# Kernel optimization log

Hardware: AMD Instinct MI355X
Metric: run time of the kernel (lower is better)

Reference implementation:

```python
import jax, jax.numpy as jnp
import numpy as np

TEMPERATURE = 8.0  # sqrt(d_k=64)
NEG_FILL = -1000.0


def setup_inputs() -> dict:
    key = jax.random.key(0)
    k1, k2, k3, k4 = jax.random.split(key, 4)
    B, Lq, Lk, D = 16, 2048, 2048, 64
    q = jax.random.normal(k1, (B, Lq, D), dtype=jnp.float32)
    k = jax.random.normal(k2, (B, Lk, D), dtype=jnp.float32)
    v = jax.random.normal(k3, (B, Lk, D), dtype=jnp.float32)
    pad_mask = jax.random.randint(k4, (B, Lk), 0, 2).astype(bool)
    return {"q": q, "k": k, "v": v, "pad_mask": pad_mask}


def reference(q, k, v, pad_mask):
    # scores: [B, Lq, Lk]
    attn = jnp.einsum('bqd,bkd->bqk', q, k) / TEMPERATURE
    # mask padded keys (broadcast over query dim, like pad_mask.unsqueeze(1))
    attn = jnp.where(pad_mask[:, None, :], NEG_FILL, attn)
    attn = jax.nn.softmax(attn, axis=-1)
    # dropout is identity in eval / p=0
    output = jnp.einsum('bqk,bkd->bqd', attn, v)
    return output, attn
```

## Files before the change

kernel.cpp:

```cpp
#include <hip/hip_runtime.h>
#include <hip/hip_bf16.h>

#define BB 16
#define LL 2048
#define DD 64

typedef __attribute__((ext_vector_type(8))) short short8t;
typedef __attribute__((ext_vector_type(4))) float f32x4;
typedef __attribute__((ext_vector_type(4))) unsigned short ushort4t;

__device__ __forceinline__ unsigned short f2bf(float x) {
  union { float f; unsigned int u; } c; c.f = x;
  unsigned int u = c.u;
  u += 0x7fffu + ((u >> 16) & 1u);
  return (unsigned short)(u >> 16);
}

__global__ void cvt_bf16(const float* __restrict__ in, unsigned short* __restrict__ out) {
  int i = (blockIdx.x * 256 + threadIdx.x) * 4;
  float4 v = *(const float4*)(in + i);
  ushort4t o;
  o.x = f2bf(v.x); o.y = f2bf(v.y); o.z = f2bf(v.z); o.w = f2bf(v.w);
  *(ushort4t*)(out + i) = o;
}

__global__ void vtrans(const float* __restrict__ v, unsigned short* __restrict__ vt) {
  __shared__ unsigned short t[64][66];
  int b = blockIdx.x >> 5, j0 = (blockIdx.x & 31) * 64;
  const float* src = v + ((size_t)b * LL + j0) * DD;
#pragma unroll
  for (int i = 0; i < 16; ++i) {
    int lin = i * 256 + threadIdx.x;
    int j = lin >> 6, d = lin & 63;
    t[j][d] = f2bf(src[lin]);
  }
  __syncthreads();
  unsigned short* dst = vt + (size_t)b * DD * LL;
#pragma unroll
  for (int i = 0; i < 16; ++i) {
    int lin = i * 256 + threadIdx.x;
    int d = lin >> 6, j = lin & 63;
    dst[(size_t)d * LL + j0 + j] = t[j][d];
  }
}

__device__ __forceinline__ void async_cp16(const unsigned short* src, unsigned short* dst_lds) {
  __builtin_amdgcn_global_load_lds(
      (const __attribute__((address_space(1))) unsigned int*)src,
      (__attribute__((address_space(3))) unsigned int*)dst_lds, 16, 0, 0);
}

__global__ void __launch_bounds__(256, 2)
attn_main(const unsigned short* __restrict__ Qb, const unsigned short* __restrict__ Kb,
          const unsigned short* __restrict__ VTb, const int* __restrict__ mask,
          float* __restrict__ out, float* __restrict__ attn) {
  __shared__ __align__(16) unsigned short TB[4][10240];
  float* redF = (float*)&TB[0][6144];
  float* rinvF = redF + 256;

  const int tid = threadIdx.x;
  const int w = tid >> 6;
  const int l = tid & 63;
  const int l15 = l & 15;
  const int g = l >> 4;

  const int swzb = (blockIdx.x & 7) * 64 + (blockIdx.x >> 3);
  const int b = swzb >> 5;
  const int q0 = (swzb & 31) << 6;

  unsigned short* K0 = &TB[w][0];
  unsigned short* K1 = &TB[w][2048];
  unsigned short* VB = &TB[w][4096];
  float* PF = (float*)&TB[w][6144];

  const unsigned short* Kbb = Kb + (size_t)b * LL * DD;
  const unsigned short* VTbb = VTb + (size_t)b * DD * LL;
  const int* maskb = mask + b * LL;

  auto loadK = [&](int k0, unsigned short* KB) {
    const unsigned short* gs = Kbb + (size_t)k0 * DD;
#pragma unroll
    for (int i2 = 0; i2 < 4; ++i2) {
      int row = i2 * 8 + (l >> 3);
      int ce = (l & 7) * 8;
      async_cp16(gs + row * 64 + (ce ^ ((row & 3) << 4)), KB + i2 * 512);
    }
  };
  auto loadV = [&](int k0) {
    const unsigned short* gs = VTbb + k0;
#pragma unroll
    for (int i2 = 0; i2 < 4; ++i2) {
      int row = i2 * 16 + (l >> 2);
      int ce = (l & 3) * 8;
      async_cp16(gs + (size_t)row * LL + (ce ^ ((row & 1) << 4)), VB + i2 * 512);
    }
  };

  short8t qf[4][2];
  {
    const unsigned short* qbase = Qb + ((size_t)b * LL + q0 + l15) * DD + 8 * g;
#pragma unroll
    for (int mi = 0; mi < 4; ++mi)
#pragma unroll
      for (int h = 0; h < 2; ++h)
        qf[mi][h] = *(const short8t*)(qbase + mi * 16 * DD + 32 * h);
  }

  float ls[4][4];
#pragma unroll
  for (int mi = 0; mi < 4; ++mi)
#pragma unroll
    for (int r = 0; r < 4; ++r) ls[mi][r] = 0.f;

  auto stepA = [&](int t, int tn, unsigned short* KBc, unsigned short* KBn,
                   int mk0c, int mk1c, int& mk0n, int& mk1n) {
    asm volatile("s_waitcnt vmcnt(0)" ::: "memory");
    loadK(tn * 32, KBn);
    mk0n = maskb[tn * 32 + l15];
    mk1n = maskb[tn * 32 + 16 + l15];

    short8t kf[2][2];
#pragma unroll
    for (int ni = 0; ni < 2; ++ni)
#pragma unroll
      for (int h = 0; h < 2; ++h) {
        int row = 16 * ni + l15;
        int col = (32 * h + 8 * g) ^ ((l15 & 3) << 4);
        kf[ni][h] = *(const short8t*)(KBc + row * 64 + col);
      }

    f32x4 sacc[4][2] = {};
    __builtin_amdgcn_s_setprio(1);
#pragma unroll
    for (int mi = 0; mi < 4; ++mi)
#pragma unroll
      for (int ni = 0; ni < 2; ++ni)
#pragma unroll
        for (int h = 0; h < 2; ++h)
          sacc[mi][ni] = __builtin_amdgcn_mfma_f32_16x16x32_bf16(qf[mi][h], kf[ni][h], sacc[mi][ni], 0, 0, 0);
    __builtin_amdgcn_s_setprio(0);
#pragma unroll
    for (int mi = 0; mi < 4; ++mi)
#pragma unroll
      for (int ni = 0; ni < 2; ++ni) {
        int mk = ni ? mk1c : mk0c;
#pragma unroll
        for (int r = 0; r < 4; ++r) {
          float p = mk ? 0.f : __expf(sacc[mi][ni][r] * 0.125f);
          ls[mi][r] += p;
        }
      }
  };

  {
    loadK(w * 32, K0);
    int a0 = maskb[w * 32 + l15], a1 = maskb[w * 32 + 16 + l15];
    int b0, b1;
    for (int j = 0; j < 8; ++j) {
      int t = w + 8 * j;
      stepA(t, t + 4, K0, K1, a0, a1, b0, b1);
      int t2 = t + 4;
      int tn = (j == 7) ? w : (t2 + 4);
      stepA(t2, tn, K1, K0, b0, b1, a0, a1);
    }
  }

#pragma unroll
  for (int mi = 0; mi < 4; ++mi)
#pragma unroll
    for (int r = 0; r < 4; ++r) {
      float s = ls[mi][r];
      s += __shfl_xor(s, 1);
      s += __shfl_xor(s, 2);
      s += __shfl_xor(s, 4);
      s += __shfl_xor(s, 8);
      if (l15 == 0) redF[w * 64 + 16 * mi + 4 * g + r] = s;
    }
  __syncthreads();
  if (tid < 64)
    rinvF[tid] = 1.0f / (redF[tid] + redF[64 + tid] + redF[128 + tid] + redF[192 + tid]);
  __syncthreads();

  float rinv_[4][4];
#pragma unroll
  for (int mi = 0; mi < 4; ++mi)
#pragma unroll
    for (int r = 0; r < 4; ++r) rinv_[mi][r] = rinvF[16 * mi + 4 * g + r];
  __syncthreads();

  f32x4 oacc[4][4] = {};
  const size_t arow = (size_t)b * LL + q0;
  auto stepB = [&](int t, int tn, const unsigned short* KBc, unsigned short* KBn,
                   int mk0c, int mk1c, int& mk0n, int& mk1n) {
    asm volatile("s_waitcnt vmcnt(8)" ::: "memory");
    const int k0 = t * 32;

    short8t kf[2][2], vf[4];
#pragma unroll
    for (int ni = 0; ni < 2; ++ni)
#pragma unroll
      for (int h = 0; h < 2; ++h) {
        int row = 16 * ni + l15;
        int col = (32 * h + 8 * g) ^ ((l15 & 3) << 4);
        kf[ni][h] = *(const short8t*)(KBc + row * 64 + col);
      }
#pragma unroll
    for (int ni = 0; ni < 4; ++ni)
      vf[ni] = *(const short8t*)(VB + (16 * ni + l15) * 32 + ((8 * g) ^ ((l & 1) << 4)));
    asm volatile("s_waitcnt lgkmcnt(0)" ::: "memory");
    __builtin_amdgcn_sched_barrier(0);

    loadK(tn * 32, KBn);
    mk0n = maskb[tn * 32 + l15];
    mk1n = maskb[tn * 32 + 16 + l15];
    loadV(tn * 32);

    f32x4 sacc[4][2] = {};
    __builtin_amdgcn_s_setprio(1);
#pragma unroll
    for (int mi = 0; mi < 4; ++mi)
#pragma unroll
      for (int ni = 0; ni < 2; ++ni)
#pragma unroll
        for (int h = 0; h < 2; ++h)
          sacc[mi][ni] = __builtin_amdgcn_mfma_f32_16x16x32_bf16(qf[mi][h], kf[ni][h], sacc[mi][ni], 0, 0, 0);
    __builtin_amdgcn_s_setprio(0);

#pragma unroll
    for (int mi = 0; mi < 4; ++mi)
#pragma unroll
      for (int ni = 0; ni < 2; ++ni) {
        int mk = ni ? mk1c : mk0c;
#pragma unroll
        for (int r = 0; r < 4; ++r) {
          float p = mk ? 0.f : __expf(sacc[mi][ni][r] * 0.125f) * rinv_[mi][r];
          PF[(16 * mi + 4 * g + r) * 32 + ((16 * ni + l15) ^ ((g & 1) << 4))] = p;
        }
      }

#pragma unroll
    for (int it = 0; it < 8; ++it) {
      int row = it * 8 + (l >> 3);
      int c4 = (l & 7) * 4;
      f32x4 pv = *(const f32x4*)(PF + row * 32 + (c4 ^ (((row >> 2) & 1) << 4)));
      __builtin_nontemporal_store(pv, (f32x4*)(attn + (arow + row) * LL + k0 + c4));
    }

    short8t pf[4];
#pragma unroll
    for (int mi = 0; mi < 4; ++mi) {
      int qq = 16 * mi + l15;
      const float* src = PF + qq * 32 + ((8 * g) ^ (((l15 >> 2) & 1) << 4));
      float4 pa = *(const float4*)(src);
      float4 pb = *(const float4*)(src + 4);
      short8t f;
      f[0] = (short)f2bf(pa.x); f[1] = (short)f2bf(pa.y);
      f[2] = (short)f2bf(pa.z); f[3] = (short)f2bf(pa.w);
      f[4] = (short)f2bf(pb.x); f[5] = (short)f2bf(pb.y);
      f[6] = (short)f2bf(pb.z); f[7] = (short)f2bf(pb.w);
      pf[mi] = f;
    }
    __builtin_amdgcn_s_setprio(1);
#pragma unroll
    for (int mi = 0; mi < 4; ++mi)
#pragma unroll
      for (int ni = 0; ni < 4; ++ni)
        oacc[mi][ni] = __builtin_amdgcn_mfma_f32_16x16x32_bf16(pf[mi], vf[ni], oacc[mi][ni], 0, 0, 0);
    __builtin_amdgcn_s_setprio(0);
  };

  {
    loadK(w * 32, K0);
    int a0 = maskb[w * 32 + l15], a1 = maskb[w * 32 + 16 + l15];
    loadV(w * 32);
    asm volatile("s_waitcnt vmcnt(0)" ::: "memory");
    int b0, b1;
    for (int j = 0; j < 8; ++j) {
      int t = w + 8 * j;
      stepB(t, t + 4, K0, K1, a0, a1, b0, b1);
      int t2 = t + 4;
      int tn = (j == 7) ? w : (t2 + 4);
      stepB(t2, tn, K1, K0, b0, b1, a0, a1);
    }
  }

  asm volatile("s_waitcnt vmcnt(0)" ::: "memory");

  __syncthreads();
  float* OB = (float*)&TB[0][0];
  if (w) {
#pragma unroll
    for (int mi = 0; mi < 4; ++mi)
#pragma unroll
      for (int ni = 0; ni < 4; ++ni)
#pragma unroll
        for (int r = 0; r < 4; ++r)
          OB[(w - 1) * 4096 + (16 * mi + 4 * g + r) * 64 + 16 * ni + l15] = oacc[mi][ni][r];
  }
  __syncthreads();
  if (w == 0) {
#pragma unroll
    for (int mi = 0; mi < 4; ++mi)
#pragma unroll
      for (int ni = 0; ni < 4; ++ni)
#pragma unroll
        for (int r = 0; r < 4; ++r) {
          int pos = (16 * mi + 4 * g + r) * 64 + 16 * ni + l15;
          OB[12288 + pos] = oacc[mi][ni][r] + OB[pos] + OB[4096 + pos] + OB[8192 + pos];
        }
  }
  __syncthreads();
#pragma unroll
  for (int it = 0; it < 4; ++it) {
    int lin = it * 256 + tid;
    int row = lin >> 4;
    int c4 = (lin & 15) * 4;
    float4 o4 = *(const float4*)(OB + 12288 + row * 64 + c4);
    *(float4*)(out + ((size_t)(b * LL + q0 + row)) * DD + c4) = o4;
  }
}

extern "C" void kernel_launch(void* const* d_in, const int* in_sizes, int n_in,
                              void* d_out, int out_size, void* d_ws, size_t ws_size,
                              hipStream_t stream) {
  const float* q = (const float*)d_in[0];
  const float* k = (const float*)d_in[1];
  const float* v = (const float*)d_in[2];
  const int* pm = (const int*)d_in[3];

  float* out = (float*)d_out;
  float* attn = out + (size_t)BB * LL * DD;

  unsigned short* Qb = (unsigned short*)d_ws;
  unsigned short* Kb = Qb + (size_t)BB * LL * DD;
  unsigned short* VT = Kb + (size_t)BB * LL * DD;

  cvt_bf16<<<2048, 256, 0, stream>>>(q, Qb);
  cvt_bf16<<<2048, 256, 0, stream>>>(k, Kb);
  vtrans<<<512, 256, 0, stream>>>(v, VT);
  attn_main<<<512, 256, 0, stream>>>(Qb, Kb, VT, pm, out, attn);
}
```

Measured before the change: 91.59 us.

## Swap MFMA operands to transpose scores, store attn directly from registers

The QK^T MFMA operands are swapped so each lane holds four consecutive keys for one query row. The mask is then loaded as int4 vectors, and row-sum reductions shrink to two cross-group shuffles. Probabilities are written straight from registers to the attn output as 16-byte stores, and packed into bf16 with the hardware v_cvt_pk_bf16_f32 instruction into a smaller padded LDS staging area for the PV MFMA. This drops the fp32 LDS round trip, the software bf16 rounding and a block barrier, and cuts LDS use. The trade-off is less coalesced global stores for attn, which now use regular stores in place of nontemporal ones.

```diff
diff --git a/kernel.cpp b/kernel.cpp
--- a/kernel.cpp
+++ b/kernel.cpp
@@ -14,6 +14,12 @@
   unsigned int u = c.u;
   u += 0x7fffu + ((u >> 16) & 1u);
   return (unsigned short)(u >> 16);
+}
+
+__device__ __forceinline__ int cvt_pk_bf16(float lo, float hi) {
+  int r;
+  asm("v_cvt_pk_bf16_f32 %0, %1, %2" : "=v"(r) : "v"(lo), "v"(hi));
+  return r;
 }
 
 __global__ void cvt_bf16(const float* __restrict__ in, unsigned short* __restrict__ out) {
@@ -54,9 +60,9 @@
 attn_main(const unsigned short* __restrict__ Qb, const unsigned short* __restrict__ Kb,
           const unsigned short* __restrict__ VTb, const int* __restrict__ mask,
           float* __restrict__ out, float* __restrict__ attn) {
-  __shared__ __align__(16) unsigned short TB[4][10240];
-  float* redF = (float*)&TB[0][6144];
-  float* rinvF = redF + 256;
+  __shared__ __align__(16) unsigned short TB[4][8704];
+  __shared__ float redF[256];
+  __shared__ float rinvF[64];
 
   const int tid = threadIdx.x;
   const int w = tid >> 6;
@@ -71,7 +77,7 @@
   unsigned short* K0 = &TB[w][0];
   unsigned short* K1 = &TB[w][2048];
   unsigned short* VB = &TB[w][4096];
-  float* PF = (float*)&TB[w][6144];
+  float* PW = (float*)&TB[w][6144];
 
   const unsigned short* Kbb = Kb + (size_t)b * LL * DD;
   const unsigned short* VTbb = VTb + (size_t)b * DD * LL;
@@ -106,18 +112,14 @@
         qf[mi][h] = *(const short8t*)(qbase + mi * 16 * DD + 32 * h);
   }
 
-  float ls[4][4];
-#pragma unroll
-  for (int mi = 0; mi < 4; ++mi)
-#pragma unroll
-    for (int r = 0; r < 4; ++r) ls[mi][r] = 0.f;
+  float ls[4] = {0.f, 0.f, 0.f, 0.f};
 
   auto stepA = [&](int t, int tn, unsigned short* KBc, unsigned short* KBn,
-                   int mk0c, int mk1c, int& mk0n, int& mk1n) {
+                   const int4& m0c, const int4& m1c, int4& m0n, int4& m1n) {
     asm volatile("s_waitcnt vmcnt(0)" ::: "memory");
     loadK(tn * 32, KBn);
-    mk0n = maskb[tn * 32 + l15];
-    mk1n = maskb[tn * 32 + 16 + l15];
+    m0n = *(const int4*)(maskb + tn * 32 + 4 * g);
+    m1n = *(const int4*)(maskb + tn * 32 + 16 + 4 * g);
 
     short8t kf[2][2];
 #pragma unroll
@@ -137,25 +139,24 @@
       for (int ni = 0; ni < 2; ++ni)
 #pragma unroll
         for (int h = 0; h < 2; ++h)
-          sacc[mi][ni] = __builtin_amdgcn_mfma_f32_16x16x32_bf16(qf[mi][h], kf[ni][h], sacc[mi][ni], 0, 0, 0);
+          sacc[mi][ni] = __builtin_amdgcn_mfma_f32_16x16x32_bf16(kf[ni][h], qf[mi][h], sacc[mi][ni], 0, 0, 0);
     __builtin_amdgcn_s_setprio(0);
 #pragma unroll
     for (int mi = 0; mi < 4; ++mi)
 #pragma unroll
       for (int ni = 0; ni < 2; ++ni) {
-        int mk = ni ? mk1c : mk0c;
-#pragma unroll
-        for (int r = 0; r < 4; ++r) {
-          float p = mk ? 0.f : __expf(sacc[mi][ni][r] * 0.125f);
-          ls[mi][r] += p;
-        }
+        const int* mk = ni ? (const int*)&m1c : (const int*)&m0c;
+#pragma unroll
+        for (int r = 0; r < 4; ++r)
+          ls[mi] += mk[r] ? 0.f : __expf(sacc[mi][ni][r] * 0.125f);
       }
   };
 
   {
     loadK(w * 32, K0);
-    int a0 = maskb[w * 32 + l15], a1 = maskb[w * 32 + 16 + l15];
-    int b0, b1;
+    int4 a0 = *(const int4*)(maskb + w * 32 + 4 * g);
+    int4 a1 = *(const int4*)(maskb + w * 32 + 16 + 4 * g);
+    int4 b0, b1;
     for (int j = 0; j < 8; ++j) {
       int t = w + 8 * j;
       stepA(t, t + 4, K0, K1, a0, a1, b0, b1);
@@ -165,33 +166,32 @@
     }
   }
 
-#pragma unroll
-  for (int mi = 0; mi < 4; ++mi)
-#pragma unroll
-    for (int r = 0; r < 4; ++r) {
-      float s = ls[mi][r];
-      s += __shfl_xor(s, 1);
-      s += __shfl_xor(s, 2);
-      s += __shfl_xor(s, 4);
-      s += __shfl_xor(s, 8);
-      if (l15 == 0) redF[w * 64 + 16 * mi + 4 * g + r] = s;
-    }
+  {
+#pragma unroll
+    for (int mi = 0; mi < 4; ++mi) {
+      float s = ls[mi];
+      s += __shfl_xor(s, 16);
+      s += __shfl_xor(s, 32);
+      ls[mi] = s;
+    }
+    if (l < 16) {
+#pragma unroll
+      for (int mi = 0; mi < 4; ++mi) redF[w * 64 + 16 * mi + l] = ls[mi];
+    }
+  }
   __syncthreads();
   if (tid < 64)
     rinvF[tid] = 1.0f / (redF[tid] + redF[64 + tid] + redF[128 + tid] + redF[192 + tid]);
   __syncthreads();
 
-  float rinv_[4][4];
-#pragma unroll
-  for (int mi = 0; mi < 4; ++mi)
-#pragma unroll
-    for (int r = 0; r < 4; ++r) rinv_[mi][r] = rinvF[16 * mi + 4 * g + r];
-  __syncthreads();
+  float rinv_[4];
+#pragma unroll
+  for (int mi = 0; mi < 4; ++mi) rinv_[mi] = rinvF[16 * mi + l15];
 
   f32x4 oacc[4][4] = {};
   const size_t arow = (size_t)b * LL + q0;
   auto stepB = [&](int t, int tn, const unsigned short* KBc, unsigned short* KBn,
-                   int mk0c, int mk1c, int& mk0n, int& mk1n) {
+                   const int4& m0c, const int4& m1c, int4& m0n, int4& m1n) {
     asm volatile("s_waitcnt vmcnt(8)" ::: "memory");
     const int k0 = t * 32;
 
@@ -211,8 +211,8 @@
     __builtin_amdgcn_sched_barrier(0);
 
     loadK(tn * 32, KBn);
-    mk0n = maskb[tn * 32 + l15];
-    mk1n = maskb[tn * 32 + 16 + l15];
+    m0n = *(const int4*)(maskb + tn * 32 + 4 * g);
+    m1n = *(const int4*)(maskb + tn * 32 + 16 + 4 * g);
     loadV(tn * 32);
 
     f32x4 sacc[4][2] = {};
@@ -223,58 +223,53 @@
       for (int ni = 0; ni < 2; ++ni)
 #pragma unroll
         for (int h = 0; h < 2; ++h)
-          sacc[mi][ni] = __builtin_amdgcn_mfma_f32_16x16x32_bf16(qf[mi][h], kf[ni][h], sacc[mi][ni], 0, 0, 0);
+          sacc[mi][ni] = __builtin_amdgcn_mfma_f32_16x16x32_bf16(kf[ni][h], qf[mi][h], sacc[mi][ni], 0, 0, 0);
     __builtin_amdgcn_s_setprio(0);
 
 #pragma unroll
-    for (int mi = 0; mi < 4; ++mi)
-#pragma unroll
-      for (int ni = 0; ni < 2; ++ni) {
-        int mk = ni ? mk1c : mk0c;
-#pragma unroll
-        for (int r = 0; r < 4; ++r) {
-          float p = mk ? 0.f : __expf(sacc[mi][ni][r] * 0.125f) * rinv_[mi][r];
-          PF[(16 * mi + 4 * g + r) * 32 + ((16 * ni + l15) ^ ((g & 1) << 4))] = p;
-        }
+    for (int mi = 0; mi < 4; ++mi) {
+      f32x4 pv0, pv1;
+#pragma unroll
+      for (int r = 0; r < 4; ++r) {
+        pv0[r] = ((const int*)&m0c)[r] ? 0.f : __expf(sacc[mi][0][r] * 0.125f) * rinv_[mi];
+        pv1[r] = ((const int*)&m1c)[r] ? 0.f : __expf(sacc[mi][1][r] * 0.125f) * rinv_[mi];
       }
-
-#pragma unroll
-    for (int it = 0; it < 8; ++it) {
-      int row = it * 8 + (l >> 3);
-      int c4 = (l & 7) * 4;
-      f32x4 pv = *(const f32x4*)(PF + row * 32 + (c4 ^ (((row >> 2) & 1) << 4)));
-      __builtin_nontemporal_store(pv, (f32x4*)(attn + (arow + row) * LL + k0 + c4));
-    }
-
-    short8t pf[4];
-#pragma unroll
-    for (int mi = 0; mi < 4; ++mi) {
-      int qq = 16 * mi + l15;
-      const float* src = PF + qq * 32 + ((8 * g) ^ (((l15 >> 2) & 1) << 4));
-      float4 pa = *(const float4*)(src);
-      float4 pb = *(const float4*)(src + 4);
-      short8t f;
-      f[0] = (short)f2bf(pa.x); f[1] = (short)f2bf(pa.y);
-      f[2] = (short)f2bf(pa.z); f[3] = (short)f2bf(pa.w);
-      f[4] = (short)f2bf(pb.x); f[5] = (short)f2bf(pb.y);
-      f[6] = (short)f2bf(pb.z); f[7] = (short)f2bf(pb.w);
-      pf[mi] = f;
-    }
+      float* dst = attn + (arow + 16 * mi + l15) * LL + k0 + 4 * g;
+      *(f32x4*)(dst) = pv0;
+      *(f32x4*)(dst + 16) = pv1;
+      int2 pa, pb;
+      pa.x = cvt_pk_bf16(pv0[0], pv0[1]);
+      pa.y = cvt_pk_bf16(pv0[2], pv0[3]);
+      pb.x = cvt_pk_bf16(pv1[0], pv1[1]);
+      pb.y = cvt_pk_bf16(pv1[2], pv1[3]);
+      float* pwm = PW + mi * 320 + l15 * 20;
+      *(int2*)(pwm + 2 * g) = pa;
+      *(int2*)(pwm + 8 + 2 * g) = pb;
+    }
+    asm volatile("s_waitcnt lgkmcnt(0)" ::: "memory");
+    __builtin_amdgcn_sched_barrier(0);
+
+    short8t pfr[4];
+#pragma unroll
+    for (int mi = 0; mi < 4; ++mi)
+      pfr[mi] = *(const short8t*)(PW + mi * 320 + l15 * 20 + 4 * g);
+
     __builtin_amdgcn_s_setprio(1);
 #pragma unroll
     for (int mi = 0; mi < 4; ++mi)
 #pragma unroll
       for (int ni = 0; ni < 4; ++ni)
-        oacc[mi][ni] = __builtin_amdgcn_mfma_f32_16x16x32_bf16(pf[mi], vf[ni], oacc[mi][ni], 0, 0, 0);
+        oacc[mi][ni] = __builtin_amdgcn_mfma_f32_16x16x32_bf16(pfr[mi], vf[ni], oacc[mi][ni], 0, 0, 0);
     __builtin_amdgcn_s_setprio(0);
   };
 
   {
     loadK(w * 32, K0);
-    int a0 = maskb[w * 32 + l15], a1 = maskb[w * 32 + 16 + l15];
+    int4 a0 = *(const int4*)(maskb + w * 32 + 4 * g);
+    int4 a1 = *(const int4*)(maskb + w * 32 + 16 + 4 * g);
     loadV(w * 32);
     asm volatile("s_waitcnt vmcnt(0)" ::: "memory");
-    int b0, b1;
+    int4 b0, b1;
     for (int j = 0; j < 8; ++j) {
       int t = w + 8 * j;
       stepB(t, t + 4, K0, K1, a0, a1, b0, b1);
```

Measured after the change: 91.55 us. About the same (-0.0%).
